# Kernel tuning notes

Measured on AMD Instinct MI355X. Metric: run time of the kernel, lower is better.

Reference implementation:

```python
import jax, jax.numpy as jnp
import numpy as np

N_NODES = 100000
N_EDGES = 1600000
N_FEATURES = 128
N_TEMPLATES = 8
N_TEMPLATE_NODES = 8
N_OUTER = 5      # outer FGW (mirror-descent) iterations
N_SINKHORN = 20  # inner Sinkhorn iterations
EPS_REL = 0.05   # entropic reg relative to mean cost magnitude


def setup_inputs() -> dict:
    key = jax.random.key(0)
    k1, k2, k3, k4, k5 = jax.random.split(key, 5)
    x = jax.random.normal(k1, (N_NODES, N_FEATURES), dtype=jnp.float32)
    edge_index = jax.random.randint(k2, (2, N_EDGES), 0, N_NODES, dtype=jnp.int32)
    templates = jax.random.normal(k3, (N_TEMPLATES, N_TEMPLATE_NODES, N_TEMPLATE_NODES), dtype=jnp.float32)
    template_features = jax.random.normal(k4, (N_TEMPLATES, N_TEMPLATE_NODES, N_FEATURES), dtype=jnp.float32)
    q0 = jax.random.normal(k5, (N_TEMPLATES, N_TEMPLATE_NODES), dtype=jnp.float32)
    alpha0 = jnp.zeros((1,), dtype=jnp.float32)
    return {"x": x, "edge_index": edge_index, "templates": templates,
            "template_features": template_features, "q0": q0, "alpha0": alpha0}


def _fgw_forward(x, edge_index, templates, template_features, q0, alpha0):
    # Fused Gromov-Wasserstein distance (square loss) between the input graph
    # (binary adjacency from edge_index, uniform node weights p) and each
    # learned template (C2=templates[k], features, weights q[k]).
    # Inner OT subproblem solved with log-domain Sinkhorn (entropic FGW).
    N, F = x.shape
    K, m, _ = templates.shape
    src, dst = edge_index[0], edge_index[1]
    alpha = jax.nn.sigmoid(alpha0)[0]          # trade-off, scalar
    q = jax.nn.softmax(q0, axis=1)             # [K, m] template node weights
    p = jnp.full((N,), 1.0 / N, dtype=x.dtype) # uniform graph node weights

    def spmm(T):
        # C1 @ T[k] for all templates using the edge list (never densify C1).
        # T: [K, N, m] -> [K, N, m]
        flat = jnp.transpose(T, (1, 0, 2)).reshape(N, K * m)
        out = jax.ops.segment_sum(flat[dst], src, num_segments=N)
        return jnp.transpose(out.reshape(N, K, m), (1, 0, 2))

    # constC for square loss: (C1^2 @ p) 1^T + 1 (C2^2 @ q)^T ; C1 binary so C1^2 = C1
    C1p = jax.ops.segment_sum(p[dst], src, num_segments=N)               # [N]
    constC = C1p[None, :, None] + jnp.einsum('kij,kj->ki', templates ** 2, q)[:, None, :]  # [K,N,m]

    # feature cost: squared euclidean  [K, N, m]
    Mfeat = (jnp.sum(x ** 2, axis=1)[None, :, None]
             + jnp.sum(template_features ** 2, axis=-1)[:, None, :]
             - 2.0 * jnp.einsum('nf,kmf->knm', x, template_features))

    logp = jnp.log(p)
    logq = jnp.log(q)

    def sinkhorn(cost):
        # log-domain Sinkhorn, batched over templates. cost: [K, N, m]
        eps = EPS_REL * jnp.mean(jnp.abs(cost), axis=(1, 2), keepdims=True)  # [K,1,1]
        e = eps[:, :, 0]  # [K,1]

        def body(carry, _):
            f, g = carry
            g = e * logq - e * jax.scipy.special.logsumexp((f[:, :, None] - cost) / eps, axis=1)
            f = e * logp[None, :] - e * jax.scipy.special.logsumexp((g[:, None, :] - cost) / eps, axis=2)
            return (f, g), None

        f0 = jnp.zeros((K, N), cost.dtype)
        g0 = jnp.zeros((K, m), cost.dtype)
        (f, g), _ = jax.lax.scan(body, (f0, g0), None, length=N_SINKHORN)
        return jnp.exp((f[:, :, None] + g[:, None, :] - cost) / eps)

    def gw_tens(T):
        # tens(T) = constC - C1 @ T @ (2*C2)^T  (square-loss GW tensor product)
        CT = spmm(T)
        return constC - 2.0 * jnp.einsum('knm,kpm->knp', CT, templates)

    def outer(T, _):
        cost = alpha * gw_tens(T) + (1.0 - alpha) * Mfeat
        return sinkhorn(cost), None

    T0 = p[None, :, None] * q[:, None, :]  # product-measure init
    T, _ = jax.lax.scan(outer, T0, None, length=N_OUTER)

    tens = gw_tens(T)
    fgw = ((1.0 - alpha) * jnp.sum(Mfeat * T, axis=(1, 2))
           + alpha * jnp.sum(tens * T, axis=(1, 2)))
    return fgw  # [K] FGW distance to each template


def reference(x, edge_index, templates, template_features, q0, alpha0):
    return _fgw_forward(x, edge_index, templates, template_features, q0, alpha0)
```

## Files before the change

kernel.cpp:

```cpp
#include <hip/hip_runtime.h>
#include <math.h>

#define NN 100000
#define NE 1600000
#define NFD 128
#define KT 8
#define MT 8
#define KM 64
#define NOUT 5
#define NSK 20
#define EPSR 0.05f

#define NBLK 248
#define RPBM 404
#define SCAN_B 391

typedef unsigned int u32;

__device__ __forceinline__ float groupmax8(float v){
  v = fmaxf(v, __shfl_xor(v,1));
  v = fmaxf(v, __shfl_xor(v,2));
  v = fmaxf(v, __shfl_xor(v,4));
  return v;
}
__device__ __forceinline__ float groupsum8(float v){
  v += __shfl_xor(v,1);
  v += __shfl_xor(v,2);
  v += __shfl_xor(v,4);
  return v;
}
__device__ __forceinline__ float ex2(float x){ return __builtin_amdgcn_exp2f(x); }
__device__ __forceinline__ float lg2(float x){ return __builtin_amdgcn_logf(x); }

__device__ __forceinline__ void gridbar(u32* cnt, u32* gen){
  __syncthreads();
  if (threadIdx.x==0){
    __builtin_amdgcn_fence(__ATOMIC_RELEASE, "agent");
    u32 g = __hip_atomic_load(gen, __ATOMIC_RELAXED, __HIP_MEMORY_SCOPE_AGENT);
    u32 old = __hip_atomic_fetch_add(cnt, 1u, __ATOMIC_RELAXED, __HIP_MEMORY_SCOPE_AGENT);
    if (old == (u32)(NBLK-1)){
      __hip_atomic_store(cnt, 0u, __ATOMIC_RELAXED, __HIP_MEMORY_SCOPE_AGENT);
      __hip_atomic_store(gen, g+1u, __ATOMIC_RELEASE, __HIP_MEMORY_SCOPE_AGENT);
    } else {
      long sp = 0;
      while (__hip_atomic_load(gen, __ATOMIC_RELAXED, __HIP_MEMORY_SCOPE_AGENT) == g){
        __builtin_amdgcn_s_sleep(1);
        if (++sp > (1L<<24)) break;
      }
    }
    __builtin_amdgcn_fence(__ATOMIC_ACQUIRE, "agent");
  }
  __syncthreads();
}

__global__ void k_prep(const float* __restrict__ tmpl, const float* __restrict__ tf,
                       const float* __restrict__ q0, const float* __restrict__ a0,
                       float* __restrict__ qbuf){
  int l = threadIdx.x;
  float z = q0[l];
  float mx = groupmax8(z);
  float ex = expf(z-mx);
  float s  = groupsum8(ex);
  float q  = ex/s;
  float lq = (z-mx) - logf(s);
  float w2q=0.f, tq=0.f;
  int base = l & 56;
  #pragma unroll
  for (int m=0;m<MT;m++){
    float qm = __shfl(q, base+m);
    float tm = tmpl[l*MT+m];
    w2q += tm*tm*qm;
    tq  += tm*qm;
  }
  qbuf[l]=q; qbuf[64+l]=lq; qbuf[128+l]=w2q; qbuf[192+l]=tq;
  if (l==0) qbuf[320] = 1.f/(1.f+expf(-a0[0]));
}

__global__ void k_deg(const int* __restrict__ src, int* __restrict__ deg){
  int i = blockIdx.x*blockDim.x + threadIdx.x;
  if (i < NE) atomicAdd(&deg[src[i]], 1);
}
__global__ void k_scan1(const int* __restrict__ deg, int* __restrict__ estart, int* __restrict__ bsum){
  __shared__ int sh[256];
  int t = threadIdx.x, b = blockIdx.x, i = b*256+t;
  int v = (i<NN)? deg[i] : 0;
  sh[t] = v; __syncthreads();
  for (int off=1; off<256; off<<=1){
    int x = (t>=off)? sh[t-off] : 0;
    __syncthreads();
    sh[t] += x;
    __syncthreads();
  }
  if (i<NN) estart[i] = sh[t]-v;
  if (t==255) bsum[b] = sh[t];
}
__global__ void k_scan2(const int* __restrict__ bsum, int* __restrict__ boff){
  __shared__ int sh[512];
  int t = threadIdx.x;
  int v = (t<SCAN_B)? bsum[t] : 0;
  sh[t]=v; __syncthreads();
  for (int off=1; off<512; off<<=1){
    int x = (t>=off)? sh[t-off] : 0;
    __syncthreads();
    sh[t]+=x;
    __syncthreads();
  }
  if (t<SCAN_B) boff[t] = sh[t]-v;
}
__global__ void k_scan3(int* __restrict__ estart, const int* __restrict__ boff){
  int i = blockIdx.x*256 + threadIdx.x;
  if (i<NN) estart[i] += boff[blockIdx.x];
}
__global__ void k_scatter(const int* __restrict__ src, const int* __restrict__ dst,
                          const int* __restrict__ estart, int* __restrict__ cnt,
                          int* __restrict__ sdst){
  int i = blockIdx.x*blockDim.x + threadIdx.x;
  if (i < NE){
    int s = src[i];
    int p = estart[s] + atomicAdd(&cnt[s],1);
    sdst[p] = dst[i];
  }
}

__global__ void __launch_bounds__(256,2) k_mfeat(const float* __restrict__ x,
                                                 const float* __restrict__ tf,
                                                 float* __restrict__ Mf){
  int t=threadIdx.x, w=t>>6, l=t&63;
  float tfr[NFD];
  #pragma unroll
  for (int j=0;j<NFD;j++) tfr[j]=tf[l*NFD+j];
  float tt=0.f;
  #pragma unroll
  for (int j=0;j<NFD;j++) tt += tfr[j]*tfr[j];
  int gw=blockIdx.x*4+w, nw=gridDim.x*4;
  for (int n=gw; n<NN; n+=nw){
    float x0=x[(size_t)n*NFD+l], x1=x[(size_t)n*NFD+64+l];
    float acc=0.f;
    #pragma unroll
    for (int j=0;j<64;j++){
      float xa=__builtin_bit_cast(float, __builtin_amdgcn_readlane(__builtin_bit_cast(int,x0), j));
      float xb=__builtin_bit_cast(float, __builtin_amdgcn_readlane(__builtin_bit_cast(int,x1), j));
      acc = fmaf(xa, tfr[j], acc);
      acc = fmaf(xb, tfr[64+j], acc);
    }
    float xx=x0*x0+x1*x1;
    xx+=__shfl_xor(xx,1); xx+=__shfl_xor(xx,2); xx+=__shfl_xor(xx,4);
    xx+=__shfl_xor(xx,8); xx+=__shfl_xor(xx,16); xx+=__shfl_xor(xx,32);
    Mf[(size_t)n*KM+l]=xx+tt-2.f*acc;
  }
}

__global__ void __launch_bounds__(1024,4) k_main(
    const float* __restrict__ tmpl, const float* __restrict__ qbuf,
    const int* __restrict__ deg, const int* __restrict__ estart,
    const int* __restrict__ sdst, const float* __restrict__ Mf,
    float* __restrict__ CT, float* __restrict__ Tg, float2* __restrict__ pb,
    float* __restrict__ absum, float* __restrict__ fgwacc,
    u32* __restrict__ cnt, u32* __restrict__ gen, float* __restrict__ outp)
{
  __shared__ float cls[RPBM*KM];
  __shared__ float shm[16*64];
  __shared__ float shs[16*64];
  __shared__ float gsh[64];

  const int t = threadIdx.x, w = t>>6, l = t&63, b = blockIdx.x;
  const int base = l&56;
  const int n0 = b*RPBM;
  const int nrows = min(RPBM, NN-n0);
  const float LOG2E = 1.4426950408889634f;
  const float logp2 = -log2f((float)NN);

  float tm[MT];
  #pragma unroll
  for (int m=0;m<MT;m++) tm[m]=tmpl[l*MT+m];
  const float w2q=qbuf[128+l], tq=qbuf[192+l], lq=qbuf[64+l], alpha=qbuf[320];
  const float onea = 1.f-alpha;

  for (int it=0; it<NOUT; ++it){
    float absacc=0.f;
    for (int rr=w; rr<nrows; rr+=16){
      int n=n0+rr;
      float c1p = (float)deg[n]*(1.f/NN);
      float mf = Mf[(size_t)n*KM+l];
      float gwt;
      if (it==0){
        gwt = c1p + w2q - 2.f*c1p*tq;
      } else {
        float ct = CT[(size_t)n*KM+l];
        float dot=0.f;
        #pragma unroll
        for(int m=0;m<MT;m++) dot += __shfl(ct, base+m)*tm[m];
        gwt = c1p + w2q - 2.f*dot;
      }
      float c = alpha*gwt + onea*mf;
      cls[rr*KM+l]=c;
      absacc += fabsf(c);
    }
    absacc = groupsum8(absacc);
    __syncthreads();
    shm[w*64+l]=absacc;
    __syncthreads();
    if (t<64 && (l&7)==0){
      float v=0.f;
      #pragma unroll
      for(int ww=0;ww<16;ww++) v+=shm[ww*64+l];
      atomicAdd(&absum[it*8+(l>>3)], v);
    }
    gridbar(cnt,gen);
    float e = EPSR * absum[it*8+(l>>3)] * (1.f/((float)NN*MT));
    float ie2 = LOG2E/e;
    for (int rr=w; rr<nrows; rr+=16) cls[rr*KM+l] *= ie2;
    __syncthreads();

    float gl2 = 0.f;
    for (int j=0;j<NSK;j++){
      float mrun=-3e38f, srun=0.f;
      for (int rr=w; rr<nrows; rr+=16){
        float c2 = cls[rr*KM+l];
        float xx;
        if (j==0){
          xx = -c2;
        } else {
          float y = gl2 - c2;
          float mx = groupmax8(y);
          float s8 = groupsum8(ex2(y-mx));
          float lse = mx + lg2(s8);
          xx = logp2 - lse - c2;
        }
        if (xx <= mrun){ srun += ex2(xx-mrun); }
        else { srun = srun*ex2(mrun-xx) + 1.f; mrun=xx; }
      }
      __syncthreads();
      shm[w*64+l]=mrun; shs[w*64+l]=srun;
      __syncthreads();
      if (t<64){
        float M=shm[l], S=shs[l];
        #pragma unroll
        for(int ww=1;ww<16;ww++){
          float m2=shm[ww*64+l], s2=shs[ww*64+l];
          float nm=fmaxf(M,m2);
          S = S*ex2(M-nm) + s2*ex2(m2-nm);
          M = nm;
        }
        pb[(size_t)(j&1)*NBLK*KM + (size_t)b*KM + l] = make_float2(M,S);
      }
      gridbar(cnt,gen);
      {
        const float2* src = pb + (size_t)(j&1)*NBLK*KM;
        float M=-3e38f, S=0.f;
        for (int bb=w; bb<NBLK; bb+=16){
          float2 v = src[(size_t)bb*KM + l];
          float nm=fmaxf(M,v.x);
          S = S*ex2(M-nm) + v.y*ex2(v.x-nm);
          M = nm;
        }
        shm[w*64+l]=M; shs[w*64+l]=S;
        __syncthreads();
        if (t<64){
          float M2=shm[l], S2=shs[l];
          #pragma unroll
          for(int ww=1;ww<16;ww++){
            float m2=shm[ww*64+l], s2=shs[ww*64+l];
            float nm=fmaxf(M2,m2);
            S2 = S2*ex2(M2-nm) + s2*ex2(m2-nm);
            M2 = nm;
          }
          float lse2 = M2 + lg2(S2);
          gsh[l] = lq*LOG2E - lse2;
        }
        __syncthreads();
        gl2 = gsh[l];
      }
    }

    for (int rr=w; rr<nrows; rr+=16){
      int n=n0+rr;
      float c2 = cls[rr*KM+l];
      float y = gl2 - c2;
      float mx = groupmax8(y);
      float s8 = groupsum8(ex2(y-mx));
      float lse = mx + lg2(s8);
      float tv = ex2(logp2 - lse + y);
      cls[rr*KM+l] = tv;
      Tg[(size_t)n*KM+l] = tv;
    }
    gridbar(cnt,gen);

    for (int rr=w; rr<nrows; rr+=16){
      int s = n0+rr;
      int st=estart[s], len=deg[s];
      float acc=0.f;
      int jj=0;
      for (; jj+3<len; jj+=4){
        int d0=sdst[st+jj], d1=sdst[st+jj+1], d2=sdst[st+jj+2], d3=sdst[st+jj+3];
        acc += Tg[(size_t)d0*KM+l]; acc += Tg[(size_t)d1*KM+l];
        acc += Tg[(size_t)d2*KM+l]; acc += Tg[(size_t)d3*KM+l];
      }
      for (; jj<len; jj++) acc += Tg[(size_t)sdst[st+jj]*KM+l];
      CT[(size_t)s*KM+l] = acc;
    }
    gridbar(cnt,gen);
  }

  float mfa=0.f, gwa=0.f;
  for (int rr=w; rr<nrows; rr+=16){
    int n=n0+rr;
    float tv = cls[rr*KM+l];
    float mf = Mf[(size_t)n*KM+l];
    float ct = CT[(size_t)n*KM+l];
    float c1p=(float)deg[n]*(1.f/NN);
    float dot=0.f;
    #pragma unroll
    for(int m=0;m<MT;m++) dot += __shfl(ct, base+m)*tm[m];
    float tens = c1p + w2q - 2.f*dot;
    mfa += mf*tv; gwa += tens*tv;
  }
  mfa=groupsum8(mfa); gwa=groupsum8(gwa);
  __syncthreads();
  shm[w*64+l]=mfa; shs[w*64+l]=gwa;
  __syncthreads();
  if (t<64 && (l&7)==0){
    float vm=0.f, vg=0.f;
    #pragma unroll
    for(int ww=0;ww<16;ww++){ vm+=shm[ww*64+l]; vg+=shs[ww*64+l]; }
    atomicAdd(&fgwacc[l>>3], vm);
    atomicAdd(&fgwacc[8+(l>>3)], vg);
  }
  gridbar(cnt,gen);
  if (b==0 && t<8){
    outp[t] = onea*fgwacc[t] + alpha*fgwacc[8+t];
  }
}

extern "C" void kernel_launch(void* const* d_in, const int* in_sizes, int n_in,
                              void* d_out, int out_size, void* d_ws, size_t ws_size,
                              hipStream_t stream){
  const float* x    = (const float*)d_in[0];
  const int*   ei   = (const int*)  d_in[1];
  const float* tmpl = (const float*)d_in[2];
  const float* tf   = (const float*)d_in[3];
  const float* q0   = (const float*)d_in[4];
  const float* a0   = (const float*)d_in[5];
  const int* src = ei;
  const int* dst = ei + NE;

  char* ws = (char*)d_ws;
  size_t o=0;
  auto carve = [&](size_t bytes)->void*{ void* p = ws+o; o += (bytes+255)&~(size_t)255; return p; };
  float* Tg    = (float*)carve((size_t)NN*KM*4);
  float* CT    = (float*)carve((size_t)NN*KM*4);
  float* Mf    = (float*)carve((size_t)NN*KM*4);
  int* sdst    = (int*)carve((size_t)NE*4);
  int* deg     = (int*)carve((size_t)NN*4);
  int* estart  = (int*)carve((size_t)NN*4);
  int* scnt    = (int*)carve((size_t)NN*4);
  int* bsum    = (int*)carve(512*4);
  int* boff    = (int*)carve(512*4);
  float* qbuf  = (float*)carve(512*4);
  float* absum = (float*)carve(64*4);
  float* fgwacc= (float*)carve(64*4);
  u32* sync    = (u32*)carve(256);
  float2* pb   = (float2*)carve((size_t)2*NBLK*KM*sizeof(float2));

  hipMemsetAsync(deg,    0, NN*4,  stream);
  hipMemsetAsync(scnt,   0, NN*4,  stream);
  hipMemsetAsync(absum,  0, 64*4,  stream);
  hipMemsetAsync(fgwacc, 0, 64*4,  stream);
  hipMemsetAsync(sync,   0, 256,   stream);

  k_prep<<<1,64,0,stream>>>(tmpl, tf, q0, a0, qbuf);
  k_deg<<<(NE+255)/256,256,0,stream>>>(src, deg);
  k_scan1<<<SCAN_B,256,0,stream>>>(deg, estart, bsum);
  k_scan2<<<1,512,0,stream>>>(bsum, boff);
  k_scan3<<<SCAN_B,256,0,stream>>>(estart, boff);
  k_scatter<<<(NE+255)/256,256,0,stream>>>(src, dst, estart, scnt, sdst);
  k_mfeat<<<512,256,0,stream>>>(x, tf, Mf);

  k_main<<<NBLK,1024,0,stream>>>(tmpl, qbuf, deg, estart, sdst, Mf,
                                 CT, Tg, pb, absum, fgwacc,
                                 sync, sync+64, (float*)d_out);
}
```

Before: 3.271 ms.

## Replace counter grid barrier with per-block flags and keep CT in registers

Replaces the atomic counter/generation grid barrier with per-block monotonic flags that every block polls in parallel, and skips the release/acquire fences on barriers whose data travels through atomics. The SpMM result CT now stays in per-thread registers (26 fixed slots), which removes the global CT buffer and one grid barrier per outer iteration. Row loops become fully unrolled slot loops, and the online log-sum-exp uses a branchless update. Edge ranks are recorded during the degree count, so the scatter kernel needs no second atomic pass. The risks are higher register pressure from the unrolled slots, and correctness that now rests on relaxed-atomic ordering.

```diff
diff --git a/kernel.cpp b/kernel.cpp
--- a/kernel.cpp
+++ b/kernel.cpp
@@ -13,9 +13,11 @@
 
 #define NBLK 248
 #define RPBM 404
+#define SLOTS 26
 #define SCAN_B 391
 
 typedef unsigned int u32;
+typedef unsigned long long u64;
 
 __device__ __forceinline__ float groupmax8(float v){
   v = fmaxf(v, __shfl_xor(v,1));
@@ -32,25 +34,32 @@
 __device__ __forceinline__ float ex2(float x){ return __builtin_amdgcn_exp2f(x); }
 __device__ __forceinline__ float lg2(float x){ return __builtin_amdgcn_logf(x); }
 
-__device__ __forceinline__ void gridbar(u32* cnt, u32* gen){
+__device__ __forceinline__ u64 packMS(float M, float S){
+  return ((u64)__builtin_bit_cast(u32, S) << 32) | (u64)__builtin_bit_cast(u32, M);
+}
+__device__ __forceinline__ float unpackM(u64 v){ return __builtin_bit_cast(float, (u32)(v & 0xffffffffull)); }
+__device__ __forceinline__ float unpackS(u64 v){ return __builtin_bit_cast(float, (u32)(v >> 32)); }
+
+__device__ __forceinline__ void gbar(u32* __restrict__ flags, u32 tgt, bool full){
+  asm volatile("s_waitcnt vmcnt(0)" ::: "memory");
   __syncthreads();
-  if (threadIdx.x==0){
-    __builtin_amdgcn_fence(__ATOMIC_RELEASE, "agent");
-    u32 g = __hip_atomic_load(gen, __ATOMIC_RELAXED, __HIP_MEMORY_SCOPE_AGENT);
-    u32 old = __hip_atomic_fetch_add(cnt, 1u, __ATOMIC_RELAXED, __HIP_MEMORY_SCOPE_AGENT);
-    if (old == (u32)(NBLK-1)){
-      __hip_atomic_store(cnt, 0u, __ATOMIC_RELAXED, __HIP_MEMORY_SCOPE_AGENT);
-      __hip_atomic_store(gen, g+1u, __ATOMIC_RELEASE, __HIP_MEMORY_SCOPE_AGENT);
-    } else {
-      long sp = 0;
-      while (__hip_atomic_load(gen, __ATOMIC_RELAXED, __HIP_MEMORY_SCOPE_AGENT) == g){
-        __builtin_amdgcn_s_sleep(1);
-        if (++sp > (1L<<24)) break;
-      }
-    }
-    __builtin_amdgcn_fence(__ATOMIC_ACQUIRE, "agent");
+  const int t = threadIdx.x;
+  if (t==0){
+    if (full) __builtin_amdgcn_fence(__ATOMIC_RELEASE, "agent");
+    __hip_atomic_store(&flags[blockIdx.x], tgt, __ATOMIC_RELAXED, __HIP_MEMORY_SCOPE_AGENT);
+  }
+  if (t < NBLK){
+    int sp = 0;
+    while (__hip_atomic_load(&flags[t], __ATOMIC_RELAXED, __HIP_MEMORY_SCOPE_AGENT) < tgt){
+      __builtin_amdgcn_s_sleep(2);
+      if (++sp > (1<<20)) break;
+    }
   }
   __syncthreads();
+  if (full){
+    if (t==0) __builtin_amdgcn_fence(__ATOMIC_ACQUIRE, "agent");
+    __syncthreads();
+  }
 }
 
 __global__ void k_prep(const float* __restrict__ tmpl, const float* __restrict__ tf,
@@ -76,9 +85,9 @@
   if (l==0) qbuf[320] = 1.f/(1.f+expf(-a0[0]));
 }
 
-__global__ void k_deg(const int* __restrict__ src, int* __restrict__ deg){
+__global__ void k_deg(const int* __restrict__ src, int* __restrict__ deg, int* __restrict__ rank){
   int i = blockIdx.x*blockDim.x + threadIdx.x;
-  if (i < NE) atomicAdd(&deg[src[i]], 1);
+  if (i < NE) rank[i] = atomicAdd(&deg[src[i]], 1);
 }
 __global__ void k_scan1(const int* __restrict__ deg, int* __restrict__ estart, int* __restrict__ bsum){
   __shared__ int sh[256];
@@ -112,13 +121,11 @@
   if (i<NN) estart[i] += boff[blockIdx.x];
 }
 __global__ void k_scatter(const int* __restrict__ src, const int* __restrict__ dst,
-                          const int* __restrict__ estart, int* __restrict__ cnt,
+                          const int* __restrict__ estart, const int* __restrict__ rank,
                           int* __restrict__ sdst){
   int i = blockIdx.x*blockDim.x + threadIdx.x;
   if (i < NE){
-    int s = src[i];
-    int p = estart[s] + atomicAdd(&cnt[s],1);
-    sdst[p] = dst[i];
+    sdst[estart[src[i]] + rank[i]] = dst[i];
   }
 }
 
@@ -154,9 +161,9 @@
     const float* __restrict__ tmpl, const float* __restrict__ qbuf,
     const int* __restrict__ deg, const int* __restrict__ estart,
     const int* __restrict__ sdst, const float* __restrict__ Mf,
-    float* __restrict__ CT, float* __restrict__ Tg, float2* __restrict__ pb,
+    float* __restrict__ Tg, u64* __restrict__ pb,
     float* __restrict__ absum, float* __restrict__ fgwacc,
-    u32* __restrict__ cnt, u32* __restrict__ gen, float* __restrict__ outp)
+    u32* __restrict__ flags, float* __restrict__ outp)
 {
   __shared__ float cls[RPBM*KM];
   __shared__ float shm[16*64];
@@ -169,32 +176,41 @@
   const int nrows = min(RPBM, NN-n0);
   const float LOG2E = 1.4426950408889634f;
   const float logp2 = -log2f((float)NN);
+  u32 bar = 0;
 
   float tm[MT];
   #pragma unroll
   for (int m=0;m<MT;m++) tm[m]=tmpl[l*MT+m];
-  const float w2q=qbuf[128+l], tq=qbuf[192+l], lq=qbuf[64+l], alpha=qbuf[320];
+  const float w2q=qbuf[128+l], tq=qbuf[192+l], lq2=qbuf[64+l]*LOG2E, alpha=qbuf[320];
   const float onea = 1.f-alpha;
+
+  float ctreg[SLOTS];
+  #pragma unroll
+  for (int s=0;s<SLOTS;s++) ctreg[s]=0.f;
 
   for (int it=0; it<NOUT; ++it){
     float absacc=0.f;
-    for (int rr=w; rr<nrows; rr+=16){
-      int n=n0+rr;
-      float c1p = (float)deg[n]*(1.f/NN);
-      float mf = Mf[(size_t)n*KM+l];
-      float gwt;
-      if (it==0){
-        gwt = c1p + w2q - 2.f*c1p*tq;
-      } else {
-        float ct = CT[(size_t)n*KM+l];
-        float dot=0.f;
-        #pragma unroll
-        for(int m=0;m<MT;m++) dot += __shfl(ct, base+m)*tm[m];
-        gwt = c1p + w2q - 2.f*dot;
-      }
-      float c = alpha*gwt + onea*mf;
-      cls[rr*KM+l]=c;
-      absacc += fabsf(c);
+    #pragma unroll
+    for (int s=0;s<SLOTS;s++){
+      int rr = w + 16*s;
+      if (rr < nrows){
+        int n = n0+rr;
+        float c1p = (float)deg[n]*(1.f/NN);
+        float mf = Mf[(size_t)n*KM+l];
+        float gwt;
+        if (it==0){
+          gwt = c1p + w2q - 2.f*c1p*tq;
+        } else {
+          float ct = ctreg[s];
+          float dot=0.f;
+          #pragma unroll
+          for(int m=0;m<MT;m++) dot += __shfl(ct, base+m)*tm[m];
+          gwt = c1p + w2q - 2.f*dot;
+        }
+        float c = alpha*gwt + onea*mf;
+        cls[rr*KM+l]=c;
+        absacc += fabsf(c);
+      }
     }
     absacc = groupsum8(absacc);
     __syncthreads();
@@ -206,29 +222,45 @@
       for(int ww=0;ww<16;ww++) v+=shm[ww*64+l];
       atomicAdd(&absum[it*8+(l>>3)], v);
     }
-    gridbar(cnt,gen);
-    float e = EPSR * absum[it*8+(l>>3)] * (1.f/((float)NN*MT));
+    gbar(flags, ++bar, false);
+    float e = EPSR * __hip_atomic_load(&absum[it*8+(l>>3)], __ATOMIC_RELAXED, __HIP_MEMORY_SCOPE_AGENT)
+                   * (1.f/((float)NN*MT));
     float ie2 = LOG2E/e;
-    for (int rr=w; rr<nrows; rr+=16) cls[rr*KM+l] *= ie2;
-    __syncthreads();
+    #pragma unroll
+    for (int s=0;s<SLOTS;s++){
+      int rr = w + 16*s;
+      if (rr < nrows) cls[rr*KM+l] *= ie2;
+    }
 
     float gl2 = 0.f;
     for (int j=0;j<NSK;j++){
       float mrun=-3e38f, srun=0.f;
-      for (int rr=w; rr<nrows; rr+=16){
-        float c2 = cls[rr*KM+l];
-        float xx;
-        if (j==0){
-          xx = -c2;
-        } else {
-          float y = gl2 - c2;
-          float mx = groupmax8(y);
-          float s8 = groupsum8(ex2(y-mx));
-          float lse = mx + lg2(s8);
-          xx = logp2 - lse - c2;
-        }
-        if (xx <= mrun){ srun += ex2(xx-mrun); }
-        else { srun = srun*ex2(mrun-xx) + 1.f; mrun=xx; }
+      if (j==0){
+        #pragma unroll
+        for (int s=0;s<SLOTS;s++){
+          int rr = w + 16*s;
+          if (rr < nrows){
+            float xx = -cls[rr*KM+l];
+            float nm = fmaxf(mrun, xx);
+            srun = srun*ex2(mrun-nm) + ex2(xx-nm);
+            mrun = nm;
+          }
+        }
+      } else {
+        #pragma unroll
+        for (int s=0;s<SLOTS;s++){
+          int rr = w + 16*s;
+          if (rr < nrows){
+            float c2 = cls[rr*KM+l];
+            float y = gl2 - c2;
+            float mx = groupmax8(y);
+            float s8 = groupsum8(ex2(y-mx));
+            float xx = logp2 - (mx+lg2(s8)) - c2;
+            float nm = fmaxf(mrun, xx);
+            srun = srun*ex2(mrun-nm) + ex2(xx-nm);
+            mrun = nm;
+          }
+        }
       }
       __syncthreads();
       shm[w*64+l]=mrun; shs[w*64+l]=srun;
@@ -242,16 +274,18 @@
           S = S*ex2(M-nm) + s2*ex2(m2-nm);
           M = nm;
         }
-        pb[(size_t)(j&1)*NBLK*KM + (size_t)b*KM + l] = make_float2(M,S);
-      }
-      gridbar(cnt,gen);
+        __hip_atomic_store(&pb[(size_t)(j&1)*NBLK*KM + (size_t)b*KM + l], packMS(M,S),
+                           __ATOMIC_RELAXED, __HIP_MEMORY_SCOPE_AGENT);
+      }
+      gbar(flags, ++bar, false);
       {
-        const float2* src = pb + (size_t)(j&1)*NBLK*KM;
+        const u64* pbs = pb + (size_t)(j&1)*NBLK*KM;
         float M=-3e38f, S=0.f;
         for (int bb=w; bb<NBLK; bb+=16){
-          float2 v = src[(size_t)bb*KM + l];
-          float nm=fmaxf(M,v.x);
-          S = S*ex2(M-nm) + v.y*ex2(v.x-nm);
+          u64 v = __hip_atomic_load(&pbs[(size_t)bb*KM + l], __ATOMIC_RELAXED, __HIP_MEMORY_SCOPE_AGENT);
+          float m2=unpackM(v), s2=unpackS(v);
+          float nm=fmaxf(M,m2);
+          S = S*ex2(M-nm) + s2*ex2(m2-nm);
           M = nm;
         }
         shm[w*64+l]=M; shs[w*64+l]=S;
@@ -265,55 +299,65 @@
             S2 = S2*ex2(M2-nm) + s2*ex2(m2-nm);
             M2 = nm;
           }
-          float lse2 = M2 + lg2(S2);
-          gsh[l] = lq*LOG2E - lse2;
+          gsh[l] = lq2 - (M2 + lg2(S2));
         }
         __syncthreads();
         gl2 = gsh[l];
       }
     }
 
-    for (int rr=w; rr<nrows; rr+=16){
-      int n=n0+rr;
-      float c2 = cls[rr*KM+l];
-      float y = gl2 - c2;
-      float mx = groupmax8(y);
-      float s8 = groupsum8(ex2(y-mx));
-      float lse = mx + lg2(s8);
-      float tv = ex2(logp2 - lse + y);
-      cls[rr*KM+l] = tv;
-      Tg[(size_t)n*KM+l] = tv;
-    }
-    gridbar(cnt,gen);
-
-    for (int rr=w; rr<nrows; rr+=16){
-      int s = n0+rr;
-      int st=estart[s], len=deg[s];
-      float acc=0.f;
-      int jj=0;
-      for (; jj+3<len; jj+=4){
-        int d0=sdst[st+jj], d1=sdst[st+jj+1], d2=sdst[st+jj+2], d3=sdst[st+jj+3];
-        acc += Tg[(size_t)d0*KM+l]; acc += Tg[(size_t)d1*KM+l];
-        acc += Tg[(size_t)d2*KM+l]; acc += Tg[(size_t)d3*KM+l];
-      }
-      for (; jj<len; jj++) acc += Tg[(size_t)sdst[st+jj]*KM+l];
-      CT[(size_t)s*KM+l] = acc;
-    }
-    gridbar(cnt,gen);
+    #pragma unroll
+    for (int s=0;s<SLOTS;s++){
+      int rr = w + 16*s;
+      if (rr < nrows){
+        int n = n0+rr;
+        float c2 = cls[rr*KM+l];
+        float y = gl2 - c2;
+        float mx = groupmax8(y);
+        float s8 = groupsum8(ex2(y-mx));
+        float lse = mx + lg2(s8);
+        float tv = ex2(logp2 - lse + y);
+        cls[rr*KM+l] = tv;
+        Tg[(size_t)n*KM+l] = tv;
+      }
+    }
+    gbar(flags, ++bar, true);
+
+    #pragma unroll
+    for (int s=0;s<SLOTS;s++){
+      int rr = w + 16*s;
+      if (rr < nrows){
+        int n = n0+rr;
+        int st=estart[n], len=deg[n];
+        float acc=0.f;
+        int jj=0;
+        for (; jj+3<len; jj+=4){
+          int d0=sdst[st+jj], d1=sdst[st+jj+1], d2=sdst[st+jj+2], d3=sdst[st+jj+3];
+          acc += Tg[(size_t)d0*KM+l]; acc += Tg[(size_t)d1*KM+l];
+          acc += Tg[(size_t)d2*KM+l]; acc += Tg[(size_t)d3*KM+l];
+        }
+        for (; jj<len; jj++) acc += Tg[(size_t)sdst[st+jj]*KM+l];
+        ctreg[s]=acc;
+      }
+    }
   }
 
   float mfa=0.f, gwa=0.f;
-  for (int rr=w; rr<nrows; rr+=16){
-    int n=n0+rr;
-    float tv = cls[rr*KM+l];
-    float mf = Mf[(size_t)n*KM+l];
-    float ct = CT[(size_t)n*KM+l];
-    float c1p=(float)deg[n]*(1.f/NN);
-    float dot=0.f;
-    #pragma unroll
-    for(int m=0;m<MT;m++) dot += __shfl(ct, base+m)*tm[m];
-    float tens = c1p + w2q - 2.f*dot;
-    mfa += mf*tv; gwa += tens*tv;
+  #pragma unroll
+  for (int s=0;s<SLOTS;s++){
+    int rr = w + 16*s;
+    if (rr < nrows){
+      int n = n0+rr;
+      float tv = cls[rr*KM+l];
+      float mf = Mf[(size_t)n*KM+l];
+      float ct = ctreg[s];
+      float c1p=(float)deg[n]*(1.f/NN);
+      float dot=0.f;
+      #pragma unroll
+      for(int m=0;m<MT;m++) dot += __shfl(ct, base+m)*tm[m];
+      float tens = c1p + w2q - 2.f*dot;
+      mfa += mf*tv; gwa += tens*tv;
+    }
   }
   mfa=groupsum8(mfa); gwa=groupsum8(gwa);
   __syncthreads();
@@ -326,9 +370,11 @@
     atomicAdd(&fgwacc[l>>3], vm);
     atomicAdd(&fgwacc[8+(l>>3)], vg);
   }
-  gridbar(cnt,gen);
+  gbar(flags, ++bar, false);
   if (b==0 && t<8){
-    outp[t] = onea*fgwacc[t] + alpha*fgwacc[8+t];
+    float fm = __hip_atomic_load(&fgwacc[t],   __ATOMIC_RELAXED, __HIP_MEMORY_SCOPE_AGENT);
+    float fg = __hip_atomic_load(&fgwacc[8+t], __ATOMIC_RELAXED, __HIP_MEMORY_SCOPE_AGENT);
+    outp[t] = onea*fm + alpha*fg;
   }
 }
 
@@ -348,35 +394,32 @@
   size_t o=0;
   auto carve = [&](size_t bytes)->void*{ void* p = ws+o; o += (bytes+255)&~(size_t)255; return p; };
   float* Tg    = (float*)carve((size_t)NN*KM*4);
-  float* CT    = (float*)carve((size_t)NN*KM*4);
   float* Mf    = (float*)carve((size_t)NN*KM*4);
   int* sdst    = (int*)carve((size_t)NE*4);
+  int* rank    = (int*)carve((size_t)NE*4);
   int* deg     = (int*)carve((size_t)NN*4);
   int* estart  = (int*)carve((size_t)NN*4);
-  int* scnt    = (int*)carve((size_t)NN*4);
   int* bsum    = (int*)carve(512*4);
   int* boff    = (int*)carve(512*4);
   float* qbuf  = (float*)carve(512*4);
   float* absum = (float*)carve(64*4);
   float* fgwacc= (float*)carve(64*4);
-  u32* sync    = (u32*)carve(256);
-  float2* pb   = (float2*)carve((size_t)2*NBLK*KM*sizeof(float2));
-
-  hipMemsetAsync(deg,    0, NN*4,  stream);
-  hipMemsetAsync(scnt,   0, NN*4,  stream);
-  hipMemsetAsync(absum,  0, 64*4,  stream);
-  hipMemsetAsync(fgwacc, 0, 64*4,  stream);
-  hipMemsetAsync(sync,   0, 256,   stream);
+  u32* flags   = (u32*)carve(NBLK*4);
+  u64* pb      = (u64*)carve((size_t)2*NBLK*KM*8);
+
+  hipMemsetAsync(deg,    0, NN*4,    stream);
+  hipMemsetAsync(absum,  0, 64*4,    stream);
+  hipMemsetAsync(fgwacc, 0, 64*4,    stream);
+  hipMemsetAsync(flags,  0, NBLK*4,  stream);
 
   k_prep<<<1,64,0,stream>>>(tmpl, tf, q0, a0, qbuf);
-  k_deg<<<(NE+255)/256,256,0,stream>>>(src, deg);
+  k_deg<<<(NE+255)/256,256,0,stream>>>(src, deg, rank);
   k_scan1<<<SCAN_B,256,0,stream>>>(deg, estart, bsum);
   k_scan2<<<1,512,0,stream>>>(bsum, boff);
   k_scan3<<<SCAN_B,256,0,stream>>>(estart, boff);
-  k_scatter<<<(NE+255)/256,256,0,stream>>>(src, dst, estart, scnt, sdst);
+  k_scatter<<<(NE+255)/256,256,0,stream>>>(src, dst, estart, rank, sdst);
   k_mfeat<<<512,256,0,stream>>>(x, tf, Mf);
 
   k_main<<<NBLK,1024,0,stream>>>(tmpl, qbuf, deg, estart, sdst, Mf,
-                                 CT, Tg, pb, absum, fgwacc,
-                                 sync, sync+64, (float*)d_out);
-}
+                                 Tg, pb, absum, fgwacc, flags, (float*)d_out);
+}
```

After: 3.132 ms. 1.04x faster.
